# Kernel tuning notes

Hardware: AMD Instinct MI355X
Metric: run time of the kernel (lower is better)

Reference implementation:

```python
import jax, jax.numpy as jnp
import numpy as np
from jax import lax

B, R, L = 8, 40, 128
IN = 256           # in_size
WDIM = 2 * IN      # word_h feature dim
DREL = 15          # dep_rel_emb_size
F = 200            # num_filters
FH = FW = 3        # filter size
HID = 300          # filter_factory_hidden

leaky = lambda x: jax.nn.leaky_relu(x, 0.01)


def setup_inputs() -> dict:
    key = jax.random.key(0)
    ks = jax.random.split(key, 16)
    s = lambda fan_in: (2.0 / fan_in) ** 0.5  # kaiming-ish scale
    inp = {
        "energy": jax.random.uniform(ks[0], (B, R, L, L), jnp.float32),
        "word_h": jax.random.normal(ks[1], (B, L, WDIM), jnp.float32),
        "e1": jax.random.normal(ks[2], (B, WDIM), jnp.float32),
        "e2": jax.random.normal(ks[3], (B, WDIM), jnp.float32),
        "sent_len": jax.random.randint(ks[4], (B,), 1, L, jnp.int64 if jax.config.jax_enable_x64 else jnp.int32),
        # params
        "rel_embs": jax.random.normal(ks[5], (R, DREL), jnp.float32) * s(DREL),
        "arc_W": jax.random.normal(ks[6], (IN, 4 * IN + DREL), jnp.float32) * s(4 * IN + DREL),
        "arc_b": jnp.zeros((IN,), jnp.float32),
        "ff_W": jax.random.normal(ks[7], (HID, 4 * IN), jnp.float32) * s(4 * IN),
        "ff_b": jnp.zeros((HID,), jnp.float32),
        "fw1": jax.random.normal(ks[8], (F, IN, FH, FW, HID), jnp.float32) * s(HID),
        "fb1": jax.random.normal(ks[9], (F, IN, FH, FW), jnp.float32) * 0.02,
        "it_W": jax.random.normal(ks[10], (F, 4 * IN), jnp.float32) * s(4 * IN),
        "it_b": jnp.zeros((F,), jnp.float32),
    }
    return inp


def _forward(energy, word_h, e1, e2, rel_embs, arc_W, arc_b, ff_W, ff_b, fw1, fb1, it_W, it_b):
    # threshold mask (energy_threshold = 0.0)
    energy = jnp.where(energy < 0.0, 0.0, energy)

    # ---- get_arc_representations ----
    marginal = energy.sum(axis=1)                                  # [B,L,L]
    rel_tensor = jnp.einsum('brij,rd->bijd', energy, rel_embs)     # [B,L,L,DREL]
    # combine_two_tensors(word_h, word_h): Z[b,i,j] = [X[b,j], Y[b,i]]
    X2 = jnp.broadcast_to(word_h[:, None, :, :], (B, L, L, WDIM))
    Y2 = jnp.broadcast_to(word_h[:, :, None, :], (B, L, L, WDIM))
    dep_head = jnp.concatenate([X2, Y2], axis=-1) * marginal[..., None]  # [B,L,L,4*IN]
    all_t = jnp.concatenate([dep_head, rel_tensor], axis=-1)       # [B,L,L,4*IN+DREL]
    arc = leaky(jnp.einsum('bijk,ok->bijo', all_t, arc_W) + arc_b) # [B,L,L,IN]
    mem_bank = jnp.transpose(arc, (0, 3, 1, 2))                    # [B,IN,L,L]

    # ---- filter factory (dropout = identity at eval) ----
    inputs = jnp.concatenate([e1, e2], axis=-1)                    # [B,4*IN]
    h = leaky(inputs @ ff_W.T + ff_b)                              # [B,HID]
    filt = leaky(jnp.einsum('fdhwk,bk->bfdhw', fw1, h) + fb1)      # [B,F,IN,3,3]

    # ---- per-sample conv2d, batched via vmap ----
    def conv_one(x, w):  # x: [IN,L,L], w: [F,IN,3,3]
        return lax.conv_general_dilated(x[None], w, (1, 1), 'VALID',
                                        dimension_numbers=('NCHW', 'OIHW', 'NCHW'))[0]
    out = jax.vmap(conv_one)(mem_bank, filt)                       # [B,F,L-2,L-2]
    result = leaky(out).reshape(B, F, -1).max(axis=-1)             # adaptive max pool -> [B,F]

    transformed = leaky(inputs @ it_W.T + it_b)                    # [B,F]
    return transformed + result


def reference(energy, word_h, e1, e2, sent_len, rel_embs, arc_W, arc_b,
              ff_W, ff_b, fw1, fb1, it_W, it_b):
    del sent_len  # unused by the original forward path
    return _forward(energy, word_h, e1, e2, rel_embs, arc_W, arc_b,
                    ff_W, ff_b, fw1, fb1, it_W, it_b)
```

## Files before the change

kernel.cpp:

```cpp
#include <hip/hip_runtime.h>
#include <stdint.h>


#define LK(x) ((x) > 0.f ? (x) : 0.01f*(x))

typedef __attribute__((ext_vector_type(8))) short s16x8;
typedef __attribute__((ext_vector_type(4))) float f32x4;

__device__ __forceinline__ unsigned short f2bf(float f) {
  union { float f; unsigned int u; } v; v.f = f;
  unsigned int u = v.u;
  return (unsigned short)((u + 0x7FFFu + ((u >> 16) & 1u)) >> 16);
}

__device__ __forceinline__ void gload_lds16(const void* g, void* l) {
  __builtin_amdgcn_global_load_lds(
      (const __attribute__((address_space(1))) unsigned int*)g,
      (__attribute__((address_space(3))) unsigned int*)l, 16, 0, 0);
}

__global__ __launch_bounds__(256) void k_prep(
    const float* __restrict__ e1, const float* __restrict__ e2,
    const float* __restrict__ rel, const float* __restrict__ aW,
    const float* __restrict__ ffW, const float* __restrict__ ffb,
    const float* __restrict__ itW, const float* __restrict__ itb,
    const float* __restrict__ wh,
    unsigned short* __restrict__ whbf, unsigned short* __restrict__ aw1,
    unsigned short* __restrict__ aw2, unsigned short* __restrict__ rwt,
    float* __restrict__ hg, float* __restrict__ trans)
{
  int bid = blockIdx.x, t = threadIdx.x;
  if (bid < 16) {
    __shared__ float in_lds[1024];
    int b = bid & 7;
    for (int k = t; k < 1024; k += 256)
      in_lds[k] = (k < 512) ? e1[b*512 + k] : e2[b*512 + (k - 512)];
    __syncthreads();
    if (bid < 8) {
      for (int o = t; o < 300; o += 256) {
        const float4* wr = (const float4*)(ffW + (size_t)o*1024);
        float acc = ffb[o];
        for (int k = 0; k < 256; ++k) {
          float4 w = wr[k]; float4 v = *(const float4*)&in_lds[k*4];
          acc += w.x*v.x + w.y*v.y + w.z*v.z + w.w*v.w;
        }
        hg[b*300 + o] = LK(acc);
      }
    } else {
      for (int o = t; o < 200; o += 256) {
        const float4* wr = (const float4*)(itW + (size_t)o*1024);
        float acc = itb[o];
        for (int k = 0; k < 256; ++k) {
          float4 w = wr[k]; float4 v = *(const float4*)&in_lds[k*4];
          acc += w.x*v.x + w.y*v.y + w.z*v.z + w.w*v.w;
        }
        trans[b*200 + o] = LK(acc);
      }
    }
  } else if (bid < 80) {
    int id0 = (bid - 16)*256 + t;
    for (int v = id0; v < 131072; v += 64*256) {
      float4 x = ((const float4*)wh)[v];
      unsigned short* dst = whbf + (size_t)v*4;
      dst[0] = f2bf(x.x); dst[1] = f2bf(x.y); dst[2] = f2bf(x.z); dst[3] = f2bf(x.w);
    }
  } else if (bid < 144) {
    int id0 = (bid - 80)*256 + t;
    for (int e = id0; e < 131072; e += 64*256) {
      int o = e >> 9, k = e & 511;
      aw1[e] = f2bf(aW[(size_t)o*1039 + k]);
      aw2[e] = f2bf(aW[(size_t)o*1039 + 512 + k]);
    }
  } else {
    int o = t;
    for (int r = 0; r < 40; ++r) {
      float s = 0.f;
      for (int d = 0; d < 15; ++d) s += rel[r*15 + d] * aW[(size_t)o*1039 + 1024 + d];
      rwt[o*72 + r] = f2bf(s);
    }
    for (int r = 40; r < 72; ++r) rwt[o*72 + r] = 0;
  }
}

__global__ __launch_bounds__(256) void k_pq(
    const unsigned short* __restrict__ whbf,
    const unsigned short* __restrict__ aw1,
    const unsigned short* __restrict__ aw2,
    float* __restrict__ Pg, float* __restrict__ Qg)
{
  int bid = blockIdx.x, t = threadIdx.x;
  int g = bid >> 8;
  int wv = t >> 6, l = t & 63, lm = l & 15, hi = l >> 4;
  int tile = (bid & 255)*4 + wv;
  int ot = tile & 15, nt = tile >> 4;
  const unsigned short* A = g ? aw2 : aw1;
  float* out = g ? Qg : Pg;
  int orow = ot*16 + lm, n = nt*16 + lm;
  f32x4 acc = {0.f, 0.f, 0.f, 0.f};
  const unsigned short* ap = A + (size_t)orow*512 + hi*8;
  const unsigned short* bp = whbf + (size_t)n*512 + hi*8;
#pragma unroll
  for (int kk = 0; kk < 16; ++kk) {
    s16x8 af = *(const s16x8*)(ap + kk*32);
    s16x8 bf = *(const s16x8*)(bp + kk*32);
    acc = __builtin_amdgcn_mfma_f32_16x16x32_bf16(af, bf, acc, 0, 0, 0);
  }
#pragma unroll
  for (int r = 0; r < 4; ++r)
    out[(size_t)n*256 + ot*16 + hi*4 + r] = acc[r];
}

__global__ __launch_bounds__(256) void k_filt(
    const float* __restrict__ fw1, const float* __restrict__ fb1,
    const float* __restrict__ hg, unsigned short* __restrict__ filtX)
{
  int bid = blockIdx.x, t = threadIdx.x;
  __shared__ __align__(16) unsigned short Abuf[64*320];
  __shared__ __align__(16) unsigned short Bbuf[16*320];
  int r0 = bid*64;
  for (int idx = t; idx < 640; idx += 256) {
    int n = idx / 40, kc = idx - (idx/40)*40;
    unsigned w[4];
#pragma unroll
    for (int j = 0; j < 8; j += 2) {
      int k = kc*8 + j;
      float a = (n < 8 && k   < 300) ? hg[n*300 + k]     : 0.f;
      float b = (n < 8 && k+1 < 300) ? hg[n*300 + k + 1] : 0.f;
      w[j>>1] = (unsigned)f2bf(a) | ((unsigned)f2bf(b) << 16);
    }
    int byte = (n*640 + kc*16) ^ ((n & 7) << 4);
    *(uint4*)((char*)Bbuf + byte) = *(uint4*)w;
  }
  const float4* src = (const float4*)(fw1 + (size_t)r0*300);
  for (int i = 0; i < 19; ++i) {
    int c4 = t + i*256;
    if (c4 < 4800) {
      float4 v = src[c4];
      int row = c4 / 75, k = (c4 - row*75)*4;
      unsigned lo  = (unsigned)f2bf(v.x) | ((unsigned)f2bf(v.y) << 16);
      unsigned hi2 = (unsigned)f2bf(v.z) | ((unsigned)f2bf(v.w) << 16);
      int byte = (row*640 + k*2) ^ ((row & 7) << 4);
      *(unsigned long long*)((char*)Abuf + byte) =
          (unsigned long long)lo | ((unsigned long long)hi2 << 32);
    }
  }
  for (int idx = t; idx < 320; idx += 256) {
    int row = idx / 5, c = idx - (idx/5)*5;
    int byte = (row*640 + 600 + c*8) ^ ((row & 7) << 4);
    *(unsigned long long*)((char*)Abuf + byte) = 0ULL;
  }
  __syncthreads();
  int wv = t >> 6, l = t & 63, lm = l & 15, hi = l >> 4;
  int arow = wv*16 + lm;
  f32x4 acc = {0.f, 0.f, 0.f, 0.f};
#pragma unroll
  for (int ks = 0; ks < 10; ++ks) {
    int abyte = (arow*640 + ks*64 + hi*16) ^ ((arow & 7) << 4);
    int bbyte = (lm*640   + ks*64 + hi*16) ^ ((lm   & 7) << 4);
    s16x8 af = *(const s16x8*)((char*)Abuf + abyte);
    s16x8 bf = *(const s16x8*)((char*)Bbuf + bbyte);
    acc = __builtin_amdgcn_mfma_f32_16x16x32_bf16(af, bf, acc, 0, 0, 0);
  }
  if (lm < 8) {
#pragma unroll
    for (int r = 0; r < 4; ++r) {
      int wrow = r0 + wv*16 + hi*4 + r;
      float v = LK(acc[r] + fb1[wrow]);
      filtX[(size_t)wrow*8 + lm] = f2bf(v);
    }
  }
}

__global__ __launch_bounds__(256) void k_tr(
    const unsigned short* __restrict__ filtX,
    unsigned short* __restrict__ filtg)
{
  __shared__ unsigned short sh[8*2312];
  int bid = blockIdx.x, t = threadIdx.x;
  int dc = bid >> 5, fch = bid & 31;
  if (fch >= 25) {
    uint4 z = {0,0,0,0};
#pragma unroll
    for (int i = 0; i < 9; ++i) {
      int idx = t + i*256;
      int b = idx / 288, rem = idx - b*288;
      char* dst = (char*)filtg + ((size_t)(b*8+dc)*256 + fch*8)*576 + rem*16;
      *(uint4*)dst = z;
    }
    return;
  }
#pragma unroll
  for (int i = 0; i < 9; ++i) {
    int rr = t + i*256;
    int f_loc = rr / 288, e = rr - f_loc*288;
    int dl = e / 9, tap = e - dl*9;
    size_t wrow = (size_t)(fch*8 + f_loc)*2304 + dc*288 + e;
    uint4 v = *(const uint4*)((const char*)filtX + wrow*16);
    const unsigned short* pv = (const unsigned short*)&v;
    int base = f_loc*288 + tap*32 + dl;
#pragma unroll
    for (int b = 0; b < 8; ++b)
      sh[b*2312 + base] = pv[b];
  }
  __syncthreads();
#pragma unroll
  for (int i = 0; i < 9; ++i) {
    int idx = t + i*256;
    int b = idx / 288, rem = idx - b*288;
    uint4 v = *(const uint4*)((const char*)sh + b*4624 + rem*16);
    char* dst = (char*)filtg + ((size_t)(b*8+dc)*256 + fch*8)*576 + rem*16;
    *(uint4*)dst = v;
  }
}

__global__ __launch_bounds__(256) void k_arc(
    const float* __restrict__ energy,
    const unsigned short* __restrict__ rwt,
    const float* __restrict__ Pg, const float* __restrict__ Qg,
    const float* __restrict__ arcb,
    unsigned short* __restrict__ memb)
{
  __shared__ unsigned short Et[128*72];
  __shared__ float mpart[256];
  __shared__ float qlds[256];
  __shared__ float blds[256];
  int bid = blockIdx.x, t = threadIdx.x;
  int b = bid >> 7, i = bid & 127;
  int jj = t & 127, half = t >> 7;
  float macc = 0.f;
  for (int rr = 0; rr < 20; ++rr) {
    int r = half*20 + rr;
    float e = energy[(((size_t)b*40 + r)*128 + i)*128 + jj];
    e = fmaxf(e, 0.f);
    macc += e;
    Et[jj*72 + r] = f2bf(e);
  }
  mpart[t] = macc;
  if (t < 128) {
#pragma unroll
    for (int r = 40; r < 72; ++r) Et[t*72 + r] = 0;
  }
  qlds[t] = Qg[((size_t)(b*128 + i))*256 + t];
  blds[t] = arcb[t];
  __syncthreads();

  int wv = t >> 6, l = t & 63, lm = l & 15, hi = l >> 4;
  unsigned short* mout = memb + ((size_t)(b*128 + i))*128*256;
  for (int otl = 0; otl < 4; ++otl) {
    int ocb = (wv*4 + otl)*16;
    const unsigned short* rp = rwt + (ocb + lm)*72 + hi*8;
    s16x8 rw0 = *(const s16x8*)rp;
    s16x8 rw1 = *(const s16x8*)(rp + 32);
    int oc0 = ocb + hi*4;
    float4 q4 = *(const float4*)&qlds[oc0];
    float4 b4 = *(const float4*)&blds[oc0];
    for (int jt = 0; jt < 8; ++jt) {
      const unsigned short* ep = &Et[(jt*16 + lm)*72 + hi*8];
      s16x8 et0 = *(const s16x8*)ep;
      s16x8 et1 = *(const s16x8*)(ep + 32);
      f32x4 acc = {0.f,0.f,0.f,0.f};
      acc = __builtin_amdgcn_mfma_f32_16x16x32_bf16(rw0, et0, acc, 0, 0, 0);
      acc = __builtin_amdgcn_mfma_f32_16x16x32_bf16(rw1, et1, acc, 0, 0, 0);
      int j = jt*16 + lm;
      float m = mpart[j] + mpart[128 + j];
      float4 p4 = *(const float4*)&Pg[((size_t)(b*128 + j))*256 + oc0];
      unsigned long long pk = 0;
#pragma unroll
      for (int r = 0; r < 4; ++r) {
        float pr = (r==0)?p4.x:((r==1)?p4.y:((r==2)?p4.z:p4.w));
        float qr = (r==0)?q4.x:((r==1)?q4.y:((r==2)?q4.z:q4.w));
        float br = (r==0)?b4.x:((r==1)?b4.y:((r==2)?b4.z:b4.w));
        float v = acc[r] + m*(pr + qr) + br;
        v = LK(v);
        pk |= ((unsigned long long)f2bf(v)) << (16*r);
      }
      *(unsigned long long*)(mout + (size_t)j*256 + oc0) = pk;
    }
  }
}

__device__ __forceinline__ void stage_mem(const unsigned short* __restrict__ memb,
                                          char* dst, int b, int y0, int dc,
                                          int wv, int l)
{
  for (int c = wv; c < 33; c += 4) {
    int id = c*64 + l;
    int ky = id / 528;
    int rem = id - ky*528;
    int x = rem >> 2, s = rem & 3;
    int cs = s ^ ((x >> 1) & 3);
    int xs = (x < 128) ? x : 127;
    const char* ms = (const char*)memb +
        (((((size_t)(b*128 + y0 + ky))*128 + xs)*256) + dc*32 + cs*8)*2;
    gload_lds16(ms, dst + c*1024);
  }
}

__global__ __launch_bounds__(256, 3) void k_conv(
    const unsigned short* __restrict__ filtg,
    const unsigned short* __restrict__ memb,
    float* __restrict__ part)
{
  __shared__ __align__(16) char smem[33792];
  int t = threadIdx.x;
  int bid = (blockIdx.x & 7)*252 + (blockIdx.x >> 3);
  int yp = bid % 63;
  int tmp = bid / 63;
  int fc = tmp & 3, b = tmp >> 2;
  int y0 = yp*2;
  int wv = t >> 6, l = t & 63, lm = l & 15, hi = l >> 4;
  int wx = wv & 1, wf = wv >> 1;

  f32x4 zero = {0.f,0.f,0.f,0.f};
  f32x4 acc[2][4][2];
#pragma unroll
  for (int yb = 0; yb < 2; ++yb)
#pragma unroll
    for (int xt = 0; xt < 4; ++xt) { acc[yb][xt][0] = zero; acc[yb][xt][1] = zero; }

  const char* fb0 = (const char*)filtg +
      ((size_t)(b*8)*256 + fc*64 + wf*32 + lm)*576 + hi*16;

  for (int dc = 0; dc < 8; ++dc) {
    s16x8 freg[2][9];
    const char* fdc = fb0 + (size_t)dc*(256*576);
#pragma unroll
    for (int ft = 0; ft < 2; ++ft)
#pragma unroll
      for (int tap = 0; tap < 9; ++tap)
        freg[ft][tap] = *(const s16x8*)(fdc + ft*(16*576) + tap*64);
    stage_mem(memb, smem, b, y0, dc, wv, l);
    __syncthreads();
#pragma unroll
    for (int r = 0; r < 4; ++r) {
#pragma unroll
      for (int kx = 0; kx < 3; ++kx) {
#pragma unroll
        for (int xt = 0; xt < 4; ++xt) {
          int x = wx*64 + xt*16 + lm + kx;
          int slot = hi ^ ((x >> 1) & 3);
          s16x8 af = *(const s16x8*)(smem + ((r*132 + x)*4 + slot)*16);
          if (r <= 2) {
            acc[0][xt][0] = __builtin_amdgcn_mfma_f32_16x16x32_bf16(af, freg[0][r*3+kx], acc[0][xt][0], 0,0,0);
            acc[0][xt][1] = __builtin_amdgcn_mfma_f32_16x16x32_bf16(af, freg[1][r*3+kx], acc[0][xt][1], 0,0,0);
          }
          if (r >= 1) {
            acc[1][xt][0] = __builtin_amdgcn_mfma_f32_16x16x32_bf16(af, freg[0][(r-1)*3+kx], acc[1][xt][0], 0,0,0);
            acc[1][xt][1] = __builtin_amdgcn_mfma_f32_16x16x32_bf16(af, freg[1][(r-1)*3+kx], acc[1][xt][1], 0,0,0);
          }
        }
      }
    }
    __syncthreads();
  }

  float pm[2][2];
  pm[0][0] = pm[0][1] = pm[1][0] = pm[1][1] = -3.4e38f;
#pragma unroll
  for (int yb = 0; yb < 2; ++yb)
#pragma unroll
    for (int xt = 0; xt < 4; ++xt) {
      int xb = wx*64 + xt*16 + hi*4;
#pragma unroll
      for (int r = 0; r < 4; ++r) {
        if (xb + r < 126) {
          pm[yb][0] = fmaxf(pm[yb][0], acc[yb][xt][0][r]);
          pm[yb][1] = fmaxf(pm[yb][1], acc[yb][xt][1][r]);
        }
      }
    }
#pragma unroll
  for (int yb = 0; yb < 2; ++yb)
#pragma unroll
    for (int ft = 0; ft < 2; ++ft) {
      pm[yb][ft] = fmaxf(pm[yb][ft], __shfl_xor(pm[yb][ft], 16));
      pm[yb][ft] = fmaxf(pm[yb][ft], __shfl_xor(pm[yb][ft], 32));
    }
  float* red = (float*)smem;
  if (l < 16) {
#pragma unroll
    for (int yb = 0; yb < 2; ++yb)
#pragma unroll
      for (int ft = 0; ft < 2; ++ft)
        red[(yb*4 + wf*2 + wx)*32 + ft*16 + lm] = pm[yb][ft];
  }
  __syncthreads();
  if (t < 128) {
    int yb = t >> 6, tt = t & 63;
    int wfi = tt >> 5, fi = tt & 31;
    float v = fmaxf(red[(yb*4 + wfi*2 + 0)*32 + fi], red[(yb*4 + wfi*2 + 1)*32 + fi]);
    v = LK(v);
    part[((size_t)(b*126 + y0 + yb))*256 + fc*64 + tt] = v;
  }
}

__global__ __launch_bounds__(256) void k_final(
    const float* __restrict__ part, const float* __restrict__ trans,
    float* __restrict__ out)
{
  int bid = blockIdx.x, t = threadIdx.x;
  int b = bid >> 3, fg = bid & 7;
  int f = fg*32 + (t >> 3), ys = t & 7;
  float m = -3.4e38f;
  for (int yy = ys; yy < 126; yy += 8)
    m = fmaxf(m, part[((size_t)(b*126 + yy))*256 + f]);
  m = fmaxf(m, __shfl_xor(m, 1));
  m = fmaxf(m, __shfl_xor(m, 2));
  m = fmaxf(m, __shfl_xor(m, 4));
  if (ys == 0 && f < 200)
    out[b*200 + f] = trans[b*200 + f] + m;
}

extern "C" void kernel_launch(void* const* d_in, const int* in_sizes, int n_in,
                              void* d_out, int out_size, void* d_ws, size_t ws_size,
                              hipStream_t stream)
{
  (void)in_sizes; (void)n_in; (void)out_size; (void)ws_size;
  const float* energy = (const float*)d_in[0];
  const float* word_h = (const float*)d_in[1];
  const float* e1     = (const float*)d_in[2];
  const float* e2     = (const float*)d_in[3];
  const float* rel    = (const float*)d_in[5];
  const float* aW     = (const float*)d_in[6];
  const float* arcb   = (const float*)d_in[7];
  const float* ffW    = (const float*)d_in[8];
  const float* ffb    = (const float*)d_in[9];
  const float* fw1    = (const float*)d_in[10];
  const float* fb1    = (const float*)d_in[11];
  const float* itW    = (const float*)d_in[12];
  const float* itb    = (const float*)d_in[13];

  char* ws = (char*)d_ws;
  unsigned short* whbf  = (unsigned short*)(ws + 0);
  unsigned short* aw1   = (unsigned short*)(ws + 1048576);
  unsigned short* aw2   = (unsigned short*)(ws + 1310720);
  unsigned short* rwt   = (unsigned short*)(ws + 1572864);
  float*          hg    = (float*)(ws + 1609728);
  float*          trans = (float*)(ws + 1619328);
  float*          Pg    = (float*)(ws + 1625728);
  float*          Qg    = (float*)(ws + 2674304);
  float*          part  = (float*)(ws + 3722880);
  unsigned short* filtg = (unsigned short*)(ws + 4755072);
  unsigned short* memb  = (unsigned short*)(ws + 14454400);
  unsigned short* filtX = (unsigned short*)(ws + 81563264);

  k_prep <<<145, 256, 0, stream>>>(e1, e2, rel, aW, ffW, ffb, itW, itb, word_h,
                                   whbf, aw1, aw2, rwt, hg, trans);
  k_pq   <<<512, 256, 0, stream>>>(whbf, aw1, aw2, Pg, Qg);
  k_filt <<<7200, 256, 0, stream>>>(fw1, fb1, hg, filtX);
  k_tr   <<<256, 256, 0, stream>>>(filtX, filtg);
  k_arc  <<<1024, 256, 0, stream>>>(energy, rwt, Pg, Qg, arcb, memb);
  k_conv <<<2016, 256, 0, stream>>>(filtg, memb, part);
  k_final<<<64, 256, 0, stream>>>(part, trans, (float*)d_out);
}
```

Before: 386.9 us.

## Compute four output rows per conv block and transpose PQ MFMA output

The conv kernel now gives each block four output rows instead of two, staging six input rows per channel chunk. Each staged row and the register-held filters are reused across more MFMAs, which cuts redundant memory-bank loads and filter reloads and halves the grid. The cost is more accumulator registers and more LDS, with occupancy lowered to two blocks per CU, and clamped tail rows doing some wasted work. The k_pq MFMA operands are also swapped so output stores become contiguous along the output dimension across lanes.

Measured after the change: 366.3 us. -5.3%, faster.

```diff
diff --git a/kernel.cpp b/kernel.cpp
--- a/kernel.cpp
+++ b/kernel.cpp
@@ -103,11 +103,12 @@
   for (int kk = 0; kk < 16; ++kk) {
     s16x8 af = *(const s16x8*)(ap + kk*32);
     s16x8 bf = *(const s16x8*)(bp + kk*32);
-    acc = __builtin_amdgcn_mfma_f32_16x16x32_bf16(af, bf, acc, 0, 0, 0);
-  }
+    acc = __builtin_amdgcn_mfma_f32_16x16x32_bf16(bf, af, acc, 0, 0, 0);
+  }
+  int nb = nt*16 + hi*4, o = ot*16 + lm;
 #pragma unroll
   for (int r = 0; r < 4; ++r)
-    out[(size_t)n*256 + ot*16 + hi*4 + r] = acc[r];
+    out[(size_t)(nb + r)*256 + o] = acc[r];
 }
 
 __global__ __launch_bounds__(256) void k_filt(
@@ -279,42 +280,25 @@
   }
 }
 
-__device__ __forceinline__ void stage_mem(const unsigned short* __restrict__ memb,
-                                          char* dst, int b, int y0, int dc,
-                                          int wv, int l)
-{
-  for (int c = wv; c < 33; c += 4) {
-    int id = c*64 + l;
-    int ky = id / 528;
-    int rem = id - ky*528;
-    int x = rem >> 2, s = rem & 3;
-    int cs = s ^ ((x >> 1) & 3);
-    int xs = (x < 128) ? x : 127;
-    const char* ms = (const char*)memb +
-        (((((size_t)(b*128 + y0 + ky))*128 + xs)*256) + dc*32 + cs*8)*2;
-    gload_lds16(ms, dst + c*1024);
-  }
-}
-
-__global__ __launch_bounds__(256, 3) void k_conv(
+__global__ __launch_bounds__(256, 2) void k_conv(
     const unsigned short* __restrict__ filtg,
     const unsigned short* __restrict__ memb,
     float* __restrict__ part)
 {
-  __shared__ __align__(16) char smem[33792];
+  __shared__ __align__(16) char smem[50688];
   int t = threadIdx.x;
-  int bid = (blockIdx.x & 7)*252 + (blockIdx.x >> 3);
-  int yp = bid % 63;
-  int tmp = bid / 63;
+  int bid = (blockIdx.x & 7)*128 + (blockIdx.x >> 3);
+  int yq = bid & 31;
+  int tmp = bid >> 5;
   int fc = tmp & 3, b = tmp >> 2;
-  int y0 = yp*2;
+  int y0 = yq*4;
   int wv = t >> 6, l = t & 63, lm = l & 15, hi = l >> 4;
   int wx = wv & 1, wf = wv >> 1;
 
   f32x4 zero = {0.f,0.f,0.f,0.f};
-  f32x4 acc[2][4][2];
-#pragma unroll
-  for (int yb = 0; yb < 2; ++yb)
+  f32x4 acc[4][4][2];
+#pragma unroll
+  for (int yb = 0; yb < 4; ++yb)
 #pragma unroll
     for (int xt = 0; xt < 4; ++xt) { acc[yb][xt][0] = zero; acc[yb][xt][1] = zero; }
 
@@ -329,10 +313,23 @@
 #pragma unroll
       for (int tap = 0; tap < 9; ++tap)
         freg[ft][tap] = *(const s16x8*)(fdc + ft*(16*576) + tap*64);
-    stage_mem(memb, smem, b, y0, dc, wv, l);
+    for (int c = wv; c < 50; c += 4) {
+      int id = c*64 + l;
+      if (id < 3168) {
+        int ky = id / 528;
+        int rem = id - ky*528;
+        int x = rem >> 2, s = rem & 3;
+        int cs = s ^ ((x >> 1) & 3);
+        int xs = (x < 128) ? x : 127;
+        int row = y0 + ky; if (row > 127) row = 127;
+        const char* ms = (const char*)memb +
+            (((((size_t)(b*128 + row))*128 + xs)*256) + dc*32 + cs*8)*2;
+        gload_lds16(ms, smem + c*1024);
+      }
+    }
     __syncthreads();
 #pragma unroll
-    for (int r = 0; r < 4; ++r) {
+    for (int r = 0; r < 6; ++r) {
 #pragma unroll
       for (int kx = 0; kx < 3; ++kx) {
 #pragma unroll
@@ -340,13 +337,13 @@
           int x = wx*64 + xt*16 + lm + kx;
           int slot = hi ^ ((x >> 1) & 3);
           s16x8 af = *(const s16x8*)(smem + ((r*132 + x)*4 + slot)*16);
-          if (r <= 2) {
-            acc[0][xt][0] = __builtin_amdgcn_mfma_f32_16x16x32_bf16(af, freg[0][r*3+kx], acc[0][xt][0], 0,0,0);
-            acc[0][xt][1] = __builtin_amdgcn_mfma_f32_16x16x32_bf16(af, freg[1][r*3+kx], acc[0][xt][1], 0,0,0);
-          }
-          if (r >= 1) {
-            acc[1][xt][0] = __builtin_amdgcn_mfma_f32_16x16x32_bf16(af, freg[0][(r-1)*3+kx], acc[1][xt][0], 0,0,0);
-            acc[1][xt][1] = __builtin_amdgcn_mfma_f32_16x16x32_bf16(af, freg[1][(r-1)*3+kx], acc[1][xt][1], 0,0,0);
+#pragma unroll
+          for (int yb = 0; yb < 4; ++yb) {
+            const int ky = r - yb;
+            if (ky >= 0 && ky <= 2) {
+              acc[yb][xt][0] = __builtin_amdgcn_mfma_f32_16x16x32_bf16(af, freg[0][ky*3+kx], acc[yb][xt][0], 0,0,0);
+              acc[yb][xt][1] = __builtin_amdgcn_mfma_f32_16x16x32_bf16(af, freg[1][ky*3+kx], acc[yb][xt][1], 0,0,0);
+            }
           }
         }
       }
@@ -354,10 +351,11 @@
     __syncthreads();
   }
 
-  float pm[2][2];
-  pm[0][0] = pm[0][1] = pm[1][0] = pm[1][1] = -3.4e38f;
-#pragma unroll
-  for (int yb = 0; yb < 2; ++yb)
+  float pm[4][2];
+#pragma unroll
+  for (int yb = 0; yb < 4; ++yb) { pm[yb][0] = -3.4e38f; pm[yb][1] = -3.4e38f; }
+#pragma unroll
+  for (int yb = 0; yb < 4; ++yb)
 #pragma unroll
     for (int xt = 0; xt < 4; ++xt) {
       int xb = wx*64 + xt*16 + hi*4;
@@ -370,7 +368,7 @@
       }
     }
 #pragma unroll
-  for (int yb = 0; yb < 2; ++yb)
+  for (int yb = 0; yb < 4; ++yb)
 #pragma unroll
     for (int ft = 0; ft < 2; ++ft) {
       pm[yb][ft] = fmaxf(pm[yb][ft], __shfl_xor(pm[yb][ft], 16));
@@ -379,18 +377,20 @@
   float* red = (float*)smem;
   if (l < 16) {
 #pragma unroll
-    for (int yb = 0; yb < 2; ++yb)
+    for (int yb = 0; yb < 4; ++yb)
 #pragma unroll
       for (int ft = 0; ft < 2; ++ft)
         red[(yb*4 + wf*2 + wx)*32 + ft*16 + lm] = pm[yb][ft];
   }
   __syncthreads();
-  if (t < 128) {
+  {
     int yb = t >> 6, tt = t & 63;
     int wfi = tt >> 5, fi = tt & 31;
-    float v = fmaxf(red[(yb*4 + wfi*2 + 0)*32 + fi], red[(yb*4 + wfi*2 + 1)*32 + fi]);
-    v = LK(v);
-    part[((size_t)(b*126 + y0 + yb))*256 + fc*64 + tt] = v;
+    if (y0 + yb < 126) {
+      float v = fmaxf(red[(yb*4 + wfi*2 + 0)*32 + fi], red[(yb*4 + wfi*2 + 1)*32 + fi]);
+      v = LK(v);
+      part[((size_t)(b*126 + y0 + yb))*256 + fc*64 + tt] = v;
+    }
   }
 }
 
@@ -450,6 +450,6 @@
   k_filt <<<7200, 256, 0, stream>>>(fw1, fb1, hg, filtX);
   k_tr   <<<256, 256, 0, stream>>>(filtX, filtg);
   k_arc  <<<1024, 256, 0, stream>>>(energy, rwt, Pg, Qg, arcb, memb);
-  k_conv <<<2016, 256, 0, stream>>>(filtg, memb, part);
+  k_conv <<<1024, 256, 0, stream>>>(filtg, memb, part);
   k_final<<<64, 256, 0, stream>>>(part, trans, (float*)d_out);
 }
```
